# Kernel optimization log

Measured on AMD Instinct MI355X. Metric: run time of the kernel, lower is better.

## Reference

```python
import jax, jax.numpy as jnp
import numpy as np

N_NODES = 500_000
N_EDGES = 500_000
H = 128  # hidden_channels


def setup_inputs() -> dict:
    key = jax.random.key(0)
    k = jax.random.split(key, 8)
    z = jax.random.normal(k[0], (N_NODES, H), dtype=jnp.float32)
    edge_index = jax.random.randint(k[1], (2, N_EDGES), 0, N_NODES, dtype=jnp.int64)
    s1 = 1.0 / np.sqrt(4 * H)
    s2 = 1.0 / np.sqrt(H)
    s3 = 1.0 / np.sqrt(H // 2)
    W1 = jax.random.uniform(k[2], (4 * H, H), jnp.float32, -s1, s1)
    b1 = jax.random.uniform(k[3], (H,), jnp.float32, -s1, s1)
    W2 = jax.random.uniform(k[4], (H, H // 2), jnp.float32, -s2, s2)
    b2 = jax.random.uniform(k[5], (H // 2,), jnp.float32, -s2, s2)
    W3 = jax.random.uniform(k[6], (H // 2, 1), jnp.float32, -s3, s3)
    b3 = jax.random.uniform(k[7], (1,), jnp.float32, -s3, s3)
    return {"z": z, "edge_index": edge_index,
            "W1": W1, "b1": b1, "W2": W2, "b2": b2, "W3": W3, "b3": b3}


def reference(z, edge_index, W1, b1, W2, b2, W3, b3):
    # gather endpoint embeddings: [E, H]
    src = z[edge_index[0]]
    dst = z[edge_index[1]]
    interaction = src * dst
    difference = jnp.abs(src - dst)
    edge_repr = jnp.concatenate([src, dst, interaction, difference], axis=-1)  # [E, 4H]
    # MLP decoder (dropout = identity at eval)
    h = jax.nn.relu(edge_repr @ W1 + b1)
    h = jax.nn.relu(h @ W2 + b2)
    score = (h @ W3 + b3).squeeze(-1)  # [E]
    return score
```

## Files before the change

kernel.cpp:

```cpp
#include <hip/hip_runtime.h>
#include <stdint.h>


typedef __bf16 bf16x8 __attribute__((ext_vector_type(8)));
typedef __bf16 bf16x4 __attribute__((ext_vector_type(4)));
typedef float  f32x4  __attribute__((ext_vector_type(4)));

__global__ void prep_kernel(const float* __restrict__ W1, const float* __restrict__ W2,
                            short* __restrict__ stage1, short* __restrict__ stage2) {
    int idx = blockIdx.x * 256 + threadIdx.x;
    if (idx < 65536) {
        int k = idx >> 7, n = idx & 127;
        float v = W1[idx];
        int ntile = n >> 4, ln = n & 15;
        int kstep = k >> 5, kr = k & 31;
        int lane = (kr >> 3) * 16 + ln;
        int j = kr & 7;
        __bf16 b = (__bf16)v;
        stage1[(((ntile * 16 + kstep) * 64 + lane) << 3) + j] = *(short*)&b;
    } else if (idx < 65536 + 8192) {
        int i2 = idx - 65536;
        int k = i2 >> 6, n = i2 & 63;
        float v = W2[i2];
        int ntile = n >> 4, ln = n & 15;
        int kstep = k >> 5, kr = k & 31;
        int lane = (kr >> 3) * 16 + ln;
        int j = kr & 7;
        __bf16 b = (__bf16)v;
        stage2[(((ntile * 4 + kstep) * 64 + lane) << 3) + j] = *(short*)&b;
    }
}

__launch_bounds__(256, 4)
__global__ void link_kernel(const float* __restrict__ z,
                            const int*   __restrict__ ei,
                            const float* __restrict__ b1,
                            const float* __restrict__ b2,
                            const float* __restrict__ w3,
                            const float* __restrict__ b3,
                            const short* __restrict__ stage1,
                            const short* __restrict__ stage2,
                            float* __restrict__ out,
                            int E) {
    __shared__ __align__(16) char smem[16384];

    const int tid  = threadIdx.x;
    const int lane = tid & 63;
    const int wave = tid >> 6;
    const int ln15 = lane & 15;
    const int quad = lane >> 4;
    const int e0   = blockIdx.x * 32;

    const int c    = tid & 31;
    const int mrow = tid >> 5;
    int si[4], di[4];
    #pragma unroll
    for (int i = 0; i < 4; ++i) {
        int eg = e0 + mrow + i * 8;
        int egc = eg < E ? eg : (E - 1);
        si[i] = ei[egc];
        di[i] = ei[E + egc];
    }
    const int cc   = c >> 1;
    const int half = c & 1;
    #pragma unroll
    for (int i = 0; i < 4; ++i) {
        int m = mrow + i * 8;
        f32x4 s = *(const f32x4*)(z + (size_t)si[i] * 128 + c * 4);
        f32x4 d = *(const f32x4*)(z + (size_t)di[i] * 128 + c * 4);
        int addr = m * 256 + ((cc ^ (m & 15)) << 4) + half * 8;
        bf16x4 ps, pd;
        #pragma unroll
        for (int j = 0; j < 4; ++j) { ps[j] = (__bf16)s[j]; pd[j] = (__bf16)d[j]; }
        *(bf16x4*)(smem + addr)        = ps;
        *(bf16x4*)(smem + 8192 + addr) = pd;
    }
    __syncthreads();

    f32x4 acc[2][2];
    #pragma unroll
    for (int mt = 0; mt < 2; ++mt)
        #pragma unroll
        for (int nt = 0; nt < 2; ++nt)
            acc[mt][nt] = (f32x4){0.f, 0.f, 0.f, 0.f};

    #pragma unroll
    for (int ks4 = 0; ks4 < 4; ++ks4) {
        bf16x8 B[2][4];
        #pragma unroll
        for (int nt = 0; nt < 2; ++nt) {
            int ntile = wave * 2 + nt;
            #pragma unroll
            for (int f = 0; f < 4; ++f)
                B[nt][f] = *(const bf16x8*)(stage1 + (((ntile * 16 + f * 4 + ks4) * 64 + lane) << 3));
        }
        #pragma unroll
        for (int mt = 0; mt < 2; ++mt) {
            int m = mt * 16 + ln15;
            int off = m * 256 + (((ks4 * 4 + quad) ^ (m & 15)) << 4);
            bf16x8 sf = *(const bf16x8*)(smem + off);
            bf16x8 df = *(const bf16x8*)(smem + 8192 + off);
            bf16x8 itf, ddf;
            #pragma unroll
            for (int j = 0; j < 8; ++j) {
                float fs = (float)sf[j], fd = (float)df[j];
                itf[j] = (__bf16)(fs * fd);
                ddf[j] = (__bf16)__builtin_fabsf(fs - fd);
            }
            #pragma unroll
            for (int nt = 0; nt < 2; ++nt) {
                acc[mt][nt] = __builtin_amdgcn_mfma_f32_16x16x32_bf16(sf,  B[nt][0], acc[mt][nt], 0, 0, 0);
                acc[mt][nt] = __builtin_amdgcn_mfma_f32_16x16x32_bf16(df,  B[nt][1], acc[mt][nt], 0, 0, 0);
                acc[mt][nt] = __builtin_amdgcn_mfma_f32_16x16x32_bf16(itf, B[nt][2], acc[mt][nt], 0, 0, 0);
                acc[mt][nt] = __builtin_amdgcn_mfma_f32_16x16x32_bf16(ddf, B[nt][3], acc[mt][nt], 0, 0, 0);
            }
        }
    }
    __syncthreads();

    #pragma unroll
    for (int nt = 0; nt < 2; ++nt) {
        int n = (wave * 2 + nt) * 16 + ln15;
        float bias = b1[n];
        #pragma unroll
        for (int mt = 0; mt < 2; ++mt) {
            #pragma unroll
            for (int r = 0; r < 4; ++r) {
                int row = mt * 16 + quad * 4 + r;
                float h = acc[mt][nt][r] + bias;
                h = h > 0.f ? h : 0.f;
                int addr = row * 256 + (((n >> 3) ^ (row & 15)) << 4) + (n & 7) * 2;
                *(__bf16*)(smem + addr) = (__bf16)h;
            }
        }
    }
    __syncthreads();

    f32x4 acc2[2];
    #pragma unroll
    for (int mt = 0; mt < 2; ++mt) acc2[mt] = (f32x4){0.f, 0.f, 0.f, 0.f};

    #pragma unroll
    for (int ks = 0; ks < 4; ++ks) {
        bf16x8 b = *(const bf16x8*)(stage2 + (((wave * 4 + ks) * 64 + lane) << 3));
        #pragma unroll
        for (int mt = 0; mt < 2; ++mt) {
            int m = mt * 16 + ln15;
            int ccr = ks * 4 + quad;
            bf16x8 a = *(const bf16x8*)(smem + m * 256 + ((ccr ^ (m & 15)) << 4));
            acc2[mt] = __builtin_amdgcn_mfma_f32_16x16x32_bf16(a, b, acc2[mt], 0, 0, 0);
        }
    }
    __syncthreads();

    {
        int n2 = wave * 16 + ln15;
        float bias = b2[n2];
        #pragma unroll
        for (int mt = 0; mt < 2; ++mt) {
            #pragma unroll
            for (int r = 0; r < 4; ++r) {
                int row = mt * 16 + quad * 4 + r;
                float h = acc2[mt][r] + bias;
                h = h > 0.f ? h : 0.f;
                *(float*)(smem + row * 272 + n2 * 4) = h;
            }
        }
    }
    __syncthreads();

    if (wave == 0 && lane < 32) {
        int e = lane;
        float accf = b3[0];
        const float* h2p = (const float*)(smem + e * 272);
        #pragma unroll
        for (int kk = 0; kk < 16; ++kk) {
            f32x4 h = *(const f32x4*)(h2p + kk * 4);
            f32x4 w = *(const f32x4*)(w3 + kk * 4);
            accf += h[0] * w[0] + h[1] * w[1] + h[2] * w[2] + h[3] * w[3];
        }
        if (e0 + e < E) out[e0 + e] = accf;
    }
}

extern "C" void kernel_launch(void* const* d_in, const int* in_sizes, int n_in,
                              void* d_out, int out_size, void* d_ws, size_t ws_size,
                              hipStream_t stream) {
    const float* z  = (const float*)d_in[0];
    const int*   ei = (const int*)  d_in[1];
    const float* W1 = (const float*)d_in[2];
    const float* b1 = (const float*)d_in[3];
    const float* W2 = (const float*)d_in[4];
    const float* b2 = (const float*)d_in[5];
    const float* W3 = (const float*)d_in[6];
    const float* b3 = (const float*)d_in[7];
    float* out = (float*)d_out;

    int E = in_sizes[1] / 2;

    short* stage1 = (short*)d_ws;
    short* stage2 = stage1 + 65536;

    prep_kernel<<<288, 256, 0, stream>>>(W1, W2, stage1, stage2);

    int nblk = (E + 31) / 32;
    link_kernel<<<nblk, 256, 0, stream>>>(z, ei, b1, b2, W3, b3, stage1, stage2, out, E);
}
```

Baseline: 452.7 us.

## Enlarge block to 128 edges with 16 waves splitting M and N tiles

Each block now handles 128 edges with 1024 threads instead of 32 edges with 256 threads. The 16 waves are arranged as a 4x4 grid over M and N tiles in layer 1, and as an 8x2 grid in layer 2. Every W1 fragment fetched from global memory now serves more rows, and there are fewer blocks to schedule. In exchange, LDS use rises to 64KB per block, which limits how many blocks fit per CU, and the larger blocks synchronise at coarser barriers.

```diff
diff --git a/kernel.cpp b/kernel.cpp
--- a/kernel.cpp
+++ b/kernel.cpp
@@ -31,7 +31,7 @@
     }
 }
 
-__launch_bounds__(256, 4)
+__launch_bounds__(1024, 8)
 __global__ void link_kernel(const float* __restrict__ z,
                             const int*   __restrict__ ei,
                             const float* __restrict__ b1,
@@ -42,21 +42,21 @@
                             const short* __restrict__ stage2,
                             float* __restrict__ out,
                             int E) {
-    __shared__ __align__(16) char smem[16384];
+    __shared__ __align__(16) char smem[65536];
 
     const int tid  = threadIdx.x;
     const int lane = tid & 63;
     const int wave = tid >> 6;
     const int ln15 = lane & 15;
     const int quad = lane >> 4;
-    const int e0   = blockIdx.x * 32;
+    const int e0   = blockIdx.x * 128;
 
     const int c    = tid & 31;
     const int mrow = tid >> 5;
     int si[4], di[4];
     #pragma unroll
     for (int i = 0; i < 4; ++i) {
-        int eg = e0 + mrow + i * 8;
+        int eg = e0 + mrow + i * 32;
         int egc = eg < E ? eg : (E - 1);
         si[i] = ei[egc];
         di[i] = ei[E + egc];
@@ -65,18 +65,20 @@
     const int half = c & 1;
     #pragma unroll
     for (int i = 0; i < 4; ++i) {
-        int m = mrow + i * 8;
+        int m = mrow + i * 32;
         f32x4 s = *(const f32x4*)(z + (size_t)si[i] * 128 + c * 4);
         f32x4 d = *(const f32x4*)(z + (size_t)di[i] * 128 + c * 4);
         int addr = m * 256 + ((cc ^ (m & 15)) << 4) + half * 8;
         bf16x4 ps, pd;
         #pragma unroll
         for (int j = 0; j < 4; ++j) { ps[j] = (__bf16)s[j]; pd[j] = (__bf16)d[j]; }
-        *(bf16x4*)(smem + addr)        = ps;
-        *(bf16x4*)(smem + 8192 + addr) = pd;
-    }
-    __syncthreads();
-
+        *(bf16x4*)(smem + addr)         = ps;
+        *(bf16x4*)(smem + 32768 + addr) = pd;
+    }
+    __syncthreads();
+
+    const int mg = wave >> 2;
+    const int ng = wave & 3;
     f32x4 acc[2][2];
     #pragma unroll
     for (int mt = 0; mt < 2; ++mt)
@@ -89,17 +91,17 @@
         bf16x8 B[2][4];
         #pragma unroll
         for (int nt = 0; nt < 2; ++nt) {
-            int ntile = wave * 2 + nt;
+            int ntile = ng * 2 + nt;
             #pragma unroll
             for (int f = 0; f < 4; ++f)
                 B[nt][f] = *(const bf16x8*)(stage1 + (((ntile * 16 + f * 4 + ks4) * 64 + lane) << 3));
         }
         #pragma unroll
         for (int mt = 0; mt < 2; ++mt) {
-            int m = mt * 16 + ln15;
+            int m = (mg * 2 + mt) * 16 + ln15;
             int off = m * 256 + (((ks4 * 4 + quad) ^ (m & 15)) << 4);
             bf16x8 sf = *(const bf16x8*)(smem + off);
-            bf16x8 df = *(const bf16x8*)(smem + 8192 + off);
+            bf16x8 df = *(const bf16x8*)(smem + 32768 + off);
             bf16x8 itf, ddf;
             #pragma unroll
             for (int j = 0; j < 8; ++j) {
@@ -120,13 +122,13 @@
 
     #pragma unroll
     for (int nt = 0; nt < 2; ++nt) {
-        int n = (wave * 2 + nt) * 16 + ln15;
+        int n = (ng * 2 + nt) * 16 + ln15;
         float bias = b1[n];
         #pragma unroll
         for (int mt = 0; mt < 2; ++mt) {
             #pragma unroll
             for (int r = 0; r < 4; ++r) {
-                int row = mt * 16 + quad * 4 + r;
+                int row = (mg * 2 + mt) * 16 + quad * 4 + r;
                 float h = acc[mt][nt][r] + bias;
                 h = h > 0.f ? h : 0.f;
                 int addr = row * 256 + (((n >> 3) ^ (row & 15)) << 4) + (n & 7) * 2;
@@ -136,41 +138,42 @@
     }
     __syncthreads();
 
+    const int mt2 = wave >> 1;
+    const int ng2 = wave & 1;
     f32x4 acc2[2];
-    #pragma unroll
-    for (int mt = 0; mt < 2; ++mt) acc2[mt] = (f32x4){0.f, 0.f, 0.f, 0.f};
+    acc2[0] = (f32x4){0.f, 0.f, 0.f, 0.f};
+    acc2[1] = (f32x4){0.f, 0.f, 0.f, 0.f};
 
     #pragma unroll
     for (int ks = 0; ks < 4; ++ks) {
-        bf16x8 b = *(const bf16x8*)(stage2 + (((wave * 4 + ks) * 64 + lane) << 3));
-        #pragma unroll
-        for (int mt = 0; mt < 2; ++mt) {
-            int m = mt * 16 + ln15;
-            int ccr = ks * 4 + quad;
-            bf16x8 a = *(const bf16x8*)(smem + m * 256 + ((ccr ^ (m & 15)) << 4));
-            acc2[mt] = __builtin_amdgcn_mfma_f32_16x16x32_bf16(a, b, acc2[mt], 0, 0, 0);
-        }
-    }
-    __syncthreads();
-
-    {
-        int n2 = wave * 16 + ln15;
+        int m = mt2 * 16 + ln15;
+        int ccr = ks * 4 + quad;
+        bf16x8 a = *(const bf16x8*)(smem + m * 256 + ((ccr ^ (m & 15)) << 4));
+        #pragma unroll
+        for (int nt = 0; nt < 2; ++nt) {
+            int ntile = ng2 * 2 + nt;
+            bf16x8 b = *(const bf16x8*)(stage2 + (((ntile * 4 + ks) * 64 + lane) << 3));
+            acc2[nt] = __builtin_amdgcn_mfma_f32_16x16x32_bf16(a, b, acc2[nt], 0, 0, 0);
+        }
+    }
+    __syncthreads();
+
+    #pragma unroll
+    for (int nt = 0; nt < 2; ++nt) {
+        int n2 = (ng2 * 2 + nt) * 16 + ln15;
         float bias = b2[n2];
         #pragma unroll
-        for (int mt = 0; mt < 2; ++mt) {
-            #pragma unroll
-            for (int r = 0; r < 4; ++r) {
-                int row = mt * 16 + quad * 4 + r;
-                float h = acc2[mt][r] + bias;
-                h = h > 0.f ? h : 0.f;
-                *(float*)(smem + row * 272 + n2 * 4) = h;
-            }
-        }
-    }
-    __syncthreads();
-
-    if (wave == 0 && lane < 32) {
-        int e = lane;
+        for (int r = 0; r < 4; ++r) {
+            int row = mt2 * 16 + quad * 4 + r;
+            float h = acc2[nt][r] + bias;
+            h = h > 0.f ? h : 0.f;
+            *(float*)(smem + row * 272 + n2 * 4) = h;
+        }
+    }
+    __syncthreads();
+
+    if (tid < 128) {
+        int e = tid;
         float accf = b3[0];
         const float* h2p = (const float*)(smem + e * 272);
         #pragma unroll
@@ -203,6 +206,6 @@
 
     prep_kernel<<<288, 256, 0, stream>>>(W1, W2, stage1, stage2);
 
-    int nblk = (E + 31) / 32;
-    link_kernel<<<nblk, 256, 0, stream>>>(z, ei, b1, b2, W3, b3, stage1, stage2, out, E);
+    int nblk = (E + 127) / 128;
+    link_kernel<<<nblk, 1024, 0, stream>>>(z, ei, b1, b2, W3, b3, stage1, stage2, out, E);
 }
```

Result: slower. 779.5 us (+72.2%).
